# Optimization experiments

Measured on AMD Instinct MI355X. Metric: run time of the kernel, lower is better.

## Reference

```python
import jax, jax.numpy as jnp
import numpy as np

ALPHA = 0.0001
BETA = 0.75
K_CONST = 1.0
N_WIN = 5


def setup_inputs() -> dict:
    key = jax.random.key(0)
    x = jax.random.normal(key, (64, 56, 56, 192), dtype=jnp.float32)
    return {"x": x}


def reference(x):
    # Faithful reproduction of the (buggy) keras LRN:
    #   head = max(c - half_n, 0)
    #   tail = min(c + half_n, C)
    #   window = x_sqr[..., head : c + tail + 1]  (end clipped to C by slicing)
    C = x.shape[-1]
    half_n = N_WIN // 2
    x_sqr = x * x
    # Exclusive-prefix cumsum along channels: cs[..., j] = sum of x_sqr[..., :j]
    cs = jnp.concatenate(
        [jnp.zeros(x.shape[:-1] + (1,), x.dtype), jnp.cumsum(x_sqr, axis=-1)],
        axis=-1,
    )  # [B,H,W,C+1]
    c = np.arange(C)
    head = np.maximum(c - half_n, 0)
    tail = np.minimum(c + half_n, C)
    end = np.minimum(c + tail + 1, C)  # python slicing clips the stop index
    # windowed sum-of-squares per output channel via prefix-sum difference
    scale = cs[..., end] - cs[..., head]  # [B,H,W,C]
    scale = (scale * (ALPHA / N_WIN) + K_CONST) ** BETA
    return x / scale
```

## Files before the change

kernel.cpp:

```cpp
#include <hip/hip_runtime.h>


constexpr int   C     = 192;
constexpr int   LPP   = 16;
constexpr int   PPW   = 4;
constexpr int   WPB   = 4;
constexpr int   BLOCK = 256;
constexpr int   GRID  = 1792;
constexpr float AON   = 0.0001f / 5.0f;

typedef float f32x4 __attribute__((ext_vector_type(4)));

__device__ __forceinline__ float bperm(int byteaddr, float v) {
  return __int_as_float(__builtin_amdgcn_ds_bpermute(byteaddr, __float_as_int(v)));
}

__device__ __forceinline__ void nt_store4(float a, float b, float c, float d,
                                          float4* __restrict__ p) {
  f32x4 t = {a, b, c, d};
  __builtin_nontemporal_store(t, (f32x4*)p);
}

__device__ __forceinline__ void lrn_body(const float4 u0, const float4 u1, const float4 u2,
                                         float4* __restrict__ ob, int sub,
                                         int a0, int a1, int a2) {
  float xs[3][4] = {{u0.x, u0.y, u0.z, u0.w},
                    {u1.x, u1.y, u1.z, u1.w},
                    {u2.x, u2.y, u2.z, u2.w}};

  float q[3];
#pragma unroll
  for (int s = 0; s < 3; ++s)
    q[s] = fmaf(xs[s][0], xs[s][0],
           fmaf(xs[s][1], xs[s][1],
           fmaf(xs[s][2], xs[s][2], xs[s][3] * xs[s][3])));

  float i0 = q[0], i1 = q[1], i2 = q[2];
#pragma unroll
  for (int off = 1; off < LPP; off <<= 1) {
    const float t0 = __shfl_up(i0, off, LPP);
    const float t1 = __shfl_up(i1, off, LPP);
    const float t2 = __shfl_up(i2, off, LPP);
    if (sub >= off) { i0 += t0; i1 += t1; i2 += t2; }
  }
  const float T0 = __shfl(i0, LPP - 1, LPP);
  const float T1 = __shfl(i1, LPP - 1, LPP);
  const float T2 = __shfl(i2, LPP - 1, LPP);
  const float total = T0 + T1 + T2;
  const float E[3] = { i0 - q[0], T0 + i1 - q[1], T0 + T1 + i2 - q[2] };

  float p[3][4];
#pragma unroll
  for (int s = 0; s < 3; ++s) {
    float run = E[s];
#pragma unroll
    for (int k = 0; k < 4; ++k) { p[s][k] = run; run = fmaf(xs[s][k], xs[s][k], run); }
  }

  float hb0[3], hb1[3];
#pragma unroll
  for (int s = 0; s < 3; ++s) {
    hb0[s] = __shfl_up(p[s][2], 1, LPP);
    hb1[s] = __shfl_up(p[s][3], 1, LPP);
  }
  const float B02 = __shfl(p[0][2], LPP - 1, LPP);
  const float B03 = __shfl(p[0][3], LPP - 1, LPP);
  const float B12 = __shfl(p[1][2], LPP - 1, LPP);
  const float B13 = __shfl(p[1][3], LPP - 1, LPP);
  if (sub == 0) {
    hb0[0] = 0.0f; hb1[0] = 0.0f;
    hb0[1] = B02;  hb1[1] = B03;
    hb0[2] = B12;  hb1[2] = B13;
  }

  float ge0[4], ge1[4];
  {
    const float r00 = bperm(a0, p[0][3]), r01 = bperm(a0, p[1][3]);
    const float r10 = bperm(a1, p[0][1]), r11 = bperm(a1, p[1][1]);
    const float r20 = bperm(a1, p[0][3]), r21 = bperm(a1, p[1][3]);
    const float r30 = bperm(a2, p[0][1]), r31 = bperm(a2, p[1][1]);
    ge0[0] = (sub < 8) ? r00 : r01;
    ge0[1] = (sub < 8) ? r10 : r11;
    ge0[2] = (sub < 8) ? r20 : r21;
    ge0[3] = (sub < 7) ? r30 : r31;
    ge1[0] = bperm(a0, p[2][3]);
    ge1[1] = bperm(a1, p[2][1]);
    ge1[2] = bperm(a1, p[2][3]);
    ge1[3] = bperm(a2, p[2][1]);
  }

#pragma unroll
  for (int s = 0; s < 3; ++s) {
    float r[4];
#pragma unroll
    for (int k = 0; k < 4; ++k) {
      const float csh = (k >= 2) ? p[s][k - 2] : (k == 0 ? hb0[s] : hb1[s]);
      float cse;
      if (s == 0)      cse = ge0[k];
      else if (s == 1) cse = (4 * sub + k >= 31) ? total : ge1[k];
      else             cse = total;
      const float eps = (cse - csh) * AON;
      const float inv = fmaf(eps, fmaf(eps, fmaf(eps, -0.6015625f, 0.65625f), -0.75f), 1.0f);
      r[k] = xs[s][k] * inv;
    }
    nt_store4(r[0], r[1], r[2], r[3], &ob[16 * s + sub]);
  }
}

__global__ __launch_bounds__(BLOCK, 8) void lrn_kernel(
    const float* __restrict__ x, float* __restrict__ out, int npix) {
  const int tid  = threadIdx.x;
  const int lane = tid & 63;
  const int w    = tid >> 6;
  const int sub  = lane & 15;
  const int pl   = lane >> 4;

  const int slot   = blockIdx.x * WPB + w;
  const int nslots = gridDim.x * WPB;
  const int ngrp   = (npix + PPW - 1) / PPW;
  int nit = (ngrp - slot + nslots - 1) / nslots;
  if (nit <= 0) return;

  const int gb = lane & 48;
  const int a0 = (gb | ((2 * sub)     & 15)) << 2;
  const int a1 = (gb | ((2 * sub + 1) & 15)) << 2;
  const int a2 = (gb | ((2 * sub + 2) & 15)) << 2;

  const float4* __restrict__ xb = (const float4*)x;
  const int nclamp = npix - 1;

  int grp = slot;
  int pix = grp * PPW + pl; if (pix > nclamp) pix = nclamp;
  int fb  = pix * (C / 4) + sub;
  float4 A0 = xb[fb], A1 = xb[fb + 16], A2 = xb[fb + 32];

  for (int t = 0; t < nit; ++t) {
    const int curfb = fb;
    const int gn = grp + nslots;
    float4 B0, B1, B2;
    if (t + 1 < nit) {
      int pixn = gn * PPW + pl; if (pixn > nclamp) pixn = nclamp;
      fb = pixn * (C / 4) + sub;
      B0 = xb[fb]; B1 = xb[fb + 16]; B2 = xb[fb + 32];
    }
    float4* ob = (float4*)out + (curfb - sub);
    lrn_body(A0, A1, A2, ob, sub, a0, a1, a2);
    grp = gn;
    A0 = B0; A1 = B1; A2 = B2;
  }
}

extern "C" void kernel_launch(void* const* d_in, const int* in_sizes, int n_in,
                              void* d_out, int out_size, void* d_ws, size_t ws_size,
                              hipStream_t stream) {
  const float* x   = (const float*)d_in[0];
  float*       out = (float*)d_out;
  const int npix = in_sizes[0] / C;
  const int ngrp = (npix + PPW - 1) / PPW;
  int grid = (ngrp + WPB - 1) / WPB;
  if (grid > GRID) grid = GRID;
  lrn_kernel<<<grid, BLOCK, 0, stream>>>(x, out, npix);
}
```

Before: 266.4 us.

## Double-buffer loads with inline-asm global loads and explicit vmcnt waits

Replaces the one-ahead compiler-scheduled prefetch with a two-deep ping-pong pipeline. Loads are issued through inline-asm global_load_dwordx4 and gated by hand-placed s_waitcnt vmcnt and sched_barrier, so more memory requests stay in flight while the previous pixel group is computed. The grid drops from 1792 to 1536 blocks and the launch-bounds occupancy hint from 8 to 6 to leave registers for the extra buffer. The risks are that the vmcnt counts depend on loads and stores retiring in issue order, that one extra clamped load can be issued at the end, and that lower occupancy may cancel the added overlap.

New measurement: 264.7 us. About the same (-0.6%).

```diff
diff --git a/kernel.cpp b/kernel.cpp
--- a/kernel.cpp
+++ b/kernel.cpp
@@ -6,7 +6,7 @@
 constexpr int   PPW   = 4;
 constexpr int   WPB   = 4;
 constexpr int   BLOCK = 256;
-constexpr int   GRID  = 1792;
+constexpr int   GRID  = 1536;
 constexpr float AON   = 0.0001f / 5.0f;
 
 typedef float f32x4 __attribute__((ext_vector_type(4)));
@@ -21,7 +21,23 @@
   __builtin_nontemporal_store(t, (f32x4*)p);
 }
 
-__device__ __forceinline__ void lrn_body(const float4 u0, const float4 u1, const float4 u2,
+__device__ __forceinline__ void issue3(const float* p, f32x4& d0, f32x4& d1, f32x4& d2) {
+  asm volatile(
+      "global_load_dwordx4 %0, %3, off\n\t"
+      "global_load_dwordx4 %1, %3, off offset:256\n\t"
+      "global_load_dwordx4 %2, %3, off offset:512"
+      : "=&v"(d0), "=&v"(d1), "=&v"(d2)
+      : "v"(p)
+      : "memory");
+}
+
+__device__ __forceinline__ int fb_of(int g, int pl, int sub, int nclamp) {
+  int p = g * PPW + pl;
+  if (p > nclamp) p = nclamp;
+  return p * (C / 4) + sub;
+}
+
+__device__ __forceinline__ void lrn_body(const f32x4 u0, const f32x4 u1, const f32x4 u2,
                                          float4* __restrict__ ob, int sub,
                                          int a0, int a1, int a2) {
   float xs[3][4] = {{u0.x, u0.y, u0.z, u0.w},
@@ -107,7 +123,7 @@
   }
 }
 
-__global__ __launch_bounds__(BLOCK, 8) void lrn_kernel(
+__global__ __launch_bounds__(BLOCK, 6) void lrn_kernel(
     const float* __restrict__ x, float* __restrict__ out, int npix) {
   const int tid  = threadIdx.x;
   const int lane = tid & 63;
@@ -118,7 +134,7 @@
   const int slot   = blockIdx.x * WPB + w;
   const int nslots = gridDim.x * WPB;
   const int ngrp   = (npix + PPW - 1) / PPW;
-  int nit = (ngrp - slot + nslots - 1) / nslots;
+  const int nit    = (ngrp - slot + nslots - 1) / nslots;
   if (nit <= 0) return;
 
   const int gb = lane & 48;
@@ -126,28 +142,42 @@
   const int a1 = (gb | ((2 * sub + 1) & 15)) << 2;
   const int a2 = (gb | ((2 * sub + 2) & 15)) << 2;
 
-  const float4* __restrict__ xb = (const float4*)x;
   const int nclamp = npix - 1;
+  float4* const obase = (float4*)out;
 
-  int grp = slot;
-  int pix = grp * PPW + pl; if (pix > nclamp) pix = nclamp;
-  int fb  = pix * (C / 4) + sub;
-  float4 A0 = xb[fb], A1 = xb[fb + 16], A2 = xb[fb + 32];
+  f32x4 A0, A1, A2, B0, B1, B2;
 
-  for (int t = 0; t < nit; ++t) {
-    const int curfb = fb;
-    const int gn = grp + nslots;
-    float4 B0, B1, B2;
-    if (t + 1 < nit) {
-      int pixn = gn * PPW + pl; if (pixn > nclamp) pixn = nclamp;
-      fb = pixn * (C / 4) + sub;
-      B0 = xb[fb]; B1 = xb[fb + 16]; B2 = xb[fb + 32];
-    }
-    float4* ob = (float4*)out + (curfb - sub);
-    lrn_body(A0, A1, A2, ob, sub, a0, a1, a2);
-    grp = gn;
-    A0 = B0; A1 = B1; A2 = B2;
+  int gnext = slot;
+  int fbA = fb_of(gnext, pl, sub, nclamp); gnext += nslots;
+  issue3(x + (size_t)fbA * 4, A0, A1, A2);
+  int fbB = fb_of(gnext, pl, sub, nclamp); gnext += nslots;
+  issue3(x + (size_t)fbB * 4, B0, B1, B2);
+  asm volatile("s_waitcnt vmcnt(3)" ::: "memory");
+  __builtin_amdgcn_sched_barrier(0);
+  lrn_body(A0, A1, A2, obase + (fbA - sub), sub, a0, a1, a2);
+  int done = 1;
+
+  for (; done + 1 < nit; done += 2) {
+    fbA = fb_of(gnext, pl, sub, nclamp); gnext += nslots;
+    issue3(x + (size_t)fbA * 4, A0, A1, A2);
+    asm volatile("s_waitcnt vmcnt(6)" ::: "memory");
+    __builtin_amdgcn_sched_barrier(0);
+    lrn_body(B0, B1, B2, obase + (fbB - sub), sub, a0, a1, a2);
+
+    fbB = fb_of(gnext, pl, sub, nclamp); gnext += nslots;
+    issue3(x + (size_t)fbB * 4, B0, B1, B2);
+    asm volatile("s_waitcnt vmcnt(6)" ::: "memory");
+    __builtin_amdgcn_sched_barrier(0);
+    lrn_body(A0, A1, A2, obase + (fbA - sub), sub, a0, a1, a2);
   }
+
+  if (done < nit) {
+    asm volatile("s_waitcnt vmcnt(0)" ::: "memory");
+    __builtin_amdgcn_sched_barrier(0);
+    lrn_body(B0, B1, B2, obase + (fbB - sub), sub, a0, a1, a2);
+  }
+
+  asm volatile("s_waitcnt vmcnt(0)" ::: "memory");
 }
 
 extern "C" void kernel_launch(void* const* d_in, const int* in_sizes, int n_in,
```
